# Performance work log

Hardware: AMD Instinct MI355X
Metric: run time of the kernel (lower is better)

Reference implementation:

```python
import jax, jax.numpy as jnp
import numpy as np

B, S, H = 2, 2048, 1024
NH, HD = 16, 64  # num heads, head dim
EPS = 1e-12


def setup_inputs() -> dict:
    key = jax.random.key(0)
    ks = jax.random.split(key, 10)
    sc = 1.0 / np.sqrt(H)
    return {
        "hidden_states": jax.random.normal(ks[0], (B, S, H), jnp.float32),
        "Wq": jax.random.normal(ks[1], (H, H), jnp.float32) * sc,
        "bq": jnp.zeros((H,), jnp.float32),
        "Wk": jax.random.normal(ks[2], (H, H), jnp.float32) * sc,
        "bk": jnp.zeros((H,), jnp.float32),
        "Wv": jax.random.normal(ks[3], (H, H), jnp.float32) * sc,
        "bv": jnp.zeros((H,), jnp.float32),
        "Wo": jax.random.normal(ks[4], (H, H), jnp.float32) * sc,
        "bo": jnp.zeros((H,), jnp.float32),
        "ln_g": jnp.ones((H,), jnp.float32),
        "ln_b": jnp.zeros((H,), jnp.float32),
    }


def reference(hidden_states, Wq, bq, Wk, bk, Wv, bv, Wo, bo, ln_g, ln_b):
    x = hidden_states  # [B,S,H]
    def split_heads(t):
        return t.reshape(B, S, NH, HD).transpose(0, 2, 1, 3)  # [B,NH,S,HD]
    q = split_heads(x @ Wq.T + bq)
    k = split_heads(x @ Wk.T + bk)
    v = split_heads(x @ Wv.T + bv)
    scores = jnp.einsum("bhqd,bhkd->bhqk", q, k) / np.sqrt(HD)
    causal = jnp.tril(jnp.ones((S, S), bool))  # [S,S]
    scores = jnp.where(causal[None, None], scores, -jnp.inf)
    probs = jax.nn.softmax(scores, axis=-1)
    ctx = jnp.einsum("bhqk,bhkd->bhqd", probs, v)
    ctx = ctx.transpose(0, 2, 1, 3).reshape(B, S, H)
    attn_out = ctx @ Wo.T + bo
    y = attn_out + x
    mu = jnp.mean(y, axis=-1, keepdims=True)
    var = jnp.mean((y - mu) ** 2, axis=-1, keepdims=True)
    return (y - mu) / jnp.sqrt(var + EPS) * ln_g + ln_b
```

## Files before the change

### kernel.cpp

```cpp
#include <hip/hip_runtime.h>

#define B_  2
#define S_  2048
#define H_  1024
#define NH_ 16
#define HD_ 64
#define M_  (B_*S_)

typedef __attribute__((ext_vector_type(8))) __bf16 bf16x8;
typedef __attribute__((ext_vector_type(4))) float  f32x4;
typedef __attribute__((ext_vector_type(8))) unsigned short us8;
typedef __attribute__((ext_vector_type(4))) float  fl4;

#define GL16(g, l) __builtin_amdgcn_global_load_lds( \
    (const __attribute__((address_space(1))) unsigned int*)(g), \
    (__attribute__((address_space(3))) unsigned int*)(l), 16, 0, 0)

__device__ __forceinline__ unsigned short f2bf(float f) {
    unsigned int u = __float_as_uint(f);
    u += 0x7fffu + ((u >> 16) & 1u);
    return (unsigned short)(u >> 16);
}

__global__ __launch_bounds__(256) void cast_kernel(
    const float* __restrict__ x,
    const float* __restrict__ wq, const float* __restrict__ wk,
    const float* __restrict__ wv, const float* __restrict__ wo,
    unsigned short* __restrict__ xb, unsigned short* __restrict__ wb) {
    size_t t  = (size_t)blockIdx.x * 256 + threadIdx.x;
    size_t e0 = t * 4;
    const size_t XN = (size_t)M_ * H_;
    const float* src;
    unsigned short* dst;
    if (e0 < XN) { src = x + e0; dst = xb + e0; }
    else {
        size_t j = e0 - XN;
        int w = (int)(j >> 20);
        size_t off = j & ((1u << 20) - 1);
        const float* wp = (w == 0) ? wq : (w == 1) ? wk : (w == 2) ? wv : wo;
        src = wp + off; dst = wb + j;
    }
    fl4 v = *(const fl4*)src;
    ushort4 o;
    o.x = f2bf(v.x); o.y = f2bf(v.y); o.z = f2bf(v.z); o.w = f2bf(v.w);
    *(ushort4*)dst = o;
}

__global__ __launch_bounds__(256) void gemm_qkv(
    const unsigned short* __restrict__ xb, const unsigned short* __restrict__ wb,
    const float* __restrict__ bq, const float* __restrict__ bk,
    const float* __restrict__ bv,
    unsigned short* __restrict__ qb, unsigned short* __restrict__ kbuf,
    unsigned short* __restrict__ vT) {
    __shared__ __align__(16) unsigned short As[128 * 64];
    __shared__ __align__(16) unsigned short Bs[128 * 64];
    const int z = blockIdx.z;
    const unsigned short* W = wb + ((size_t)z << 20);
    const int m0 = blockIdx.x * 128, n0 = blockIdx.y * 128;
    const int t = threadIdx.x, lane = t & 63, w = t >> 6;
    const int wm = w >> 1, wn = w & 1, quad = lane >> 4, l16 = lane & 15;
    const int srow = w * 32 + (lane >> 3);
    const int scol = (lane & 7) * 8;
    const unsigned short* ga = xb + (size_t)(m0 + srow) * H_ + scol;
    const unsigned short* gb = W  + (size_t)(n0 + srow) * H_ + scol;

    f32x4 acc[4][4] = {};
    for (int k0 = 0; k0 < H_; k0 += 64) {
        __syncthreads();
#pragma unroll
        for (int j = 0; j < 4; j++) {
            GL16(ga + (size_t)(j * 8) * H_ + k0, &As[(w * 32 + j * 8) * 64]);
            GL16(gb + (size_t)(j * 8) * H_ + k0, &Bs[(w * 32 + j * 8) * 64]);
        }
        __syncthreads();
#pragma unroll
        for (int kk = 0; kk < 64; kk += 32) {
            bf16x8 af[4], bfr[4];
#pragma unroll
            for (int i = 0; i < 4; i++)
                af[i]  = *(const bf16x8*)&As[(wm * 64 + i * 16 + l16) * 64 + kk + quad * 8];
#pragma unroll
            for (int i = 0; i < 4; i++)
                bfr[i] = *(const bf16x8*)&Bs[(wn * 64 + i * 16 + l16) * 64 + kk + quad * 8];
#pragma unroll
            for (int mi = 0; mi < 4; mi++)
#pragma unroll
                for (int ni = 0; ni < 4; ni++)
                    acc[mi][ni] = __builtin_amdgcn_mfma_f32_16x16x32_bf16(
                        af[mi], bfr[ni], acc[mi][ni], 0, 0, 0);
        }
    }
    const float* bias = (z == 0) ? bq : (z == 1) ? bk : bv;
    if (z == 2) {
#pragma unroll
        for (int mi = 0; mi < 4; mi++) {
#pragma unroll
            for (int ni = 0; ni < 4; ni++) {
                int col  = n0 + wn * 64 + ni * 16 + l16;
                float bval = bias[col];
                int row0 = m0 + wm * 64 + mi * 16 + quad * 4;
                int bb = row0 >> 11, s0 = row0 & 2047;
                ushort4 pk;
                pk.x = f2bf(acc[mi][ni][0] + bval);
                pk.y = f2bf(acc[mi][ni][1] + bval);
                pk.z = f2bf(acc[mi][ni][2] + bval);
                pk.w = f2bf(acc[mi][ni][3] + bval);
                *(ushort4*)&vT[((size_t)bb * NH_ * HD_ + col) * S_ + s0] = pk;
            }
        }
    } else {
        unsigned short* out = (z == 0) ? qb : kbuf;
        const float qs = (z == 0) ? 0.18033688f : 1.0f;
#pragma unroll
        for (int mi = 0; mi < 4; mi++) {
#pragma unroll
            for (int ni = 0; ni < 4; ni++) {
                int col = n0 + wn * 64 + ni * 16 + l16;
                float bval = bias[col];
#pragma unroll
                for (int r = 0; r < 4; r++) {
                    int row = m0 + wm * 64 + mi * 16 + quad * 4 + r;
                    out[(size_t)row * H_ + col] = f2bf((acc[mi][ni][r] + bval) * qs);
                }
            }
        }
    }
}

__global__ __launch_bounds__(256) void gemm_out(
    const unsigned short* __restrict__ ctxb, const unsigned short* __restrict__ wob,
    const float* __restrict__ bo, const float* __restrict__ x,
    float* __restrict__ y) {
    __shared__ __align__(16) unsigned short As[128 * 64];
    __shared__ __align__(16) unsigned short Bs[64 * 64];
    const int m0 = blockIdx.x * 128, n0 = blockIdx.y * 64;
    const int t = threadIdx.x, lane = t & 63, w = t >> 6;
    const int quad = lane >> 4, l16 = lane & 15;
    const int l8r = lane >> 3, l8c = (lane & 7) * 8;
    const unsigned short* ga = ctxb + (size_t)(m0 + w * 32 + l8r) * H_ + l8c;
    const unsigned short* gb = wob  + (size_t)(n0 + w * 16 + l8r) * H_ + l8c;

    f32x4 acc[2][4] = {};
    for (int k0 = 0; k0 < H_; k0 += 64) {
        __syncthreads();
#pragma unroll
        for (int j = 0; j < 4; j++)
            GL16(ga + (size_t)(j * 8) * H_ + k0, &As[(w * 32 + j * 8) * 64]);
#pragma unroll
        for (int j = 0; j < 2; j++)
            GL16(gb + (size_t)(j * 8) * H_ + k0, &Bs[(w * 16 + j * 8) * 64]);
        __syncthreads();
#pragma unroll
        for (int kk = 0; kk < 64; kk += 32) {
            bf16x8 af[2], bfr[4];
#pragma unroll
            for (int i = 0; i < 2; i++)
                af[i]  = *(const bf16x8*)&As[(w * 32 + i * 16 + l16) * 64 + kk + quad * 8];
#pragma unroll
            for (int i = 0; i < 4; i++)
                bfr[i] = *(const bf16x8*)&Bs[(i * 16 + l16) * 64 + kk + quad * 8];
#pragma unroll
            for (int mi = 0; mi < 2; mi++)
#pragma unroll
                for (int ni = 0; ni < 4; ni++)
                    acc[mi][ni] = __builtin_amdgcn_mfma_f32_16x16x32_bf16(
                        af[mi], bfr[ni], acc[mi][ni], 0, 0, 0);
        }
    }
#pragma unroll
    for (int mi = 0; mi < 2; mi++) {
#pragma unroll
        for (int ni = 0; ni < 4; ni++) {
            int col = n0 + ni * 16 + l16;
            float bval = bo[col];
#pragma unroll
            for (int r = 0; r < 4; r++) {
                size_t idx = (size_t)(m0 + w * 32 + mi * 16 + quad * 4 + r) * H_ + col;
                y[idx] = acc[mi][ni][r] + bval + x[idx];
            }
        }
    }
}

__global__ __launch_bounds__(256) void attn_kernel(
    const unsigned short* __restrict__ qb, const unsigned short* __restrict__ kb,
    const unsigned short* __restrict__ vT, unsigned short* __restrict__ ctxb) {
    __shared__ __align__(16) unsigned short Ks[2][64 * 72];
    __shared__ __align__(16) unsigned short Vt[2][64 * 72];
    __shared__ __align__(16) unsigned short Ps[64 * 76];
    const int flat = blockIdx.x + (blockIdx.y << 4) + (blockIdx.z << 8);
    const int xcd = flat & 7, slot = flat >> 3;
    const int bh = xcd * 4 + (slot >> 4);
    const int p  = slot & 15;
    const int b = bh >> 4, h = bh & 15;
    const int t = threadIdx.x, lane = t & 63, wid = t >> 6;
    const int quad = lane >> 4, l16 = lane & 15;
    const int sr = t >> 2, sc = (t & 3) * 16;
    const size_t headoff = (size_t)h * HD_;
    const unsigned short* vtb = vT + ((size_t)(b * NH_ + h) * HD_) * S_;

    for (int half = 0; half < 2; half++) {
        const int qt = half ? (31 - p) : p;
        const int q0 = qt * 64;
        const size_t qrow = (size_t)(b * S_ + q0 + wid * 16 + l16);
        bf16x8 qf0 = *(const bf16x8*)(qb + qrow * H_ + headoff + quad * 8);
        bf16x8 qf1 = *(const bf16x8*)(qb + qrow * H_ + headoff + 32 + quad * 8);

        float m_r = -1e30f, l_r = 0.f;
        f32x4 o_acc[4] = {};

        const unsigned short* kptr = kb  + (size_t)(b * S_ + sr) * H_ + headoff + sc;
        const unsigned short* vptr = vtb + (size_t)sr * S_ + sc;
        us8 nk0 = *(const us8*)(kptr);
        us8 nk1 = *(const us8*)(kptr + 8);
        us8 nv0 = *(const us8*)(vptr);
        us8 nv1 = *(const us8*)(vptr + 8);
        __syncthreads();
        *(us8*)&Ks[0][sr * 72 + sc]     = nk0;  *(us8*)&Ks[0][sr * 72 + sc + 8] = nk1;
        *(us8*)&Vt[0][sr * 72 + sc]     = nv0;  *(us8*)&Vt[0][sr * 72 + sc + 8] = nv1;
        __syncthreads();

        for (int s = 0; s <= qt; s++) {
            const int buf = s & 1;
            const bool pf = (s < qt);
            if (pf) {
                kptr += (size_t)64 * H_;
                vptr += 64;
                nk0 = *(const us8*)(kptr);
                nk1 = *(const us8*)(kptr + 8);
                nv0 = *(const us8*)(vptr);
                nv1 = *(const us8*)(vptr + 8);
            }
            f32x4 sacc[4] = {};
#pragma unroll
            for (int kk = 0; kk < 64; kk += 32) {
                bf16x8 bq_ = (kk == 0) ? qf0 : qf1;
#pragma unroll
                for (int nt = 0; nt < 4; nt++) {
                    bf16x8 ak = *(const bf16x8*)&Ks[buf][(nt * 16 + l16) * 72 + kk + quad * 8];
                    sacc[nt] = __builtin_amdgcn_mfma_f32_16x16x32_bf16(ak, bq_, sacc[nt], 0, 0, 0);
                }
            }
            if (s == qt) {
#pragma unroll
                for (int nt = 0; nt < 4; nt++) {
#pragma unroll
                    for (int r = 0; r < 4; r++) {
                        int key = nt * 16 + quad * 4 + r;
                        if (key > wid * 16 + l16) sacc[nt][r] = -1e30f;
                    }
                }
            }
            float mx = sacc[0][0];
#pragma unroll
            for (int nt = 0; nt < 4; nt++)
#pragma unroll
                for (int r = 0; r < 4; r++) mx = fmaxf(mx, sacc[nt][r]);
            mx = fmaxf(mx, __shfl_xor(mx, 16));
            mx = fmaxf(mx, __shfl_xor(mx, 32));
            float m_new = fmaxf(m_r, mx);
            float alpha = exp2f(m_r - m_new);
            float ss = 0.f;
#pragma unroll
            for (int nt = 0; nt < 4; nt++) {
                ushort4 pk;
                float p0 = exp2f(sacc[nt][0] - m_new);
                float p1 = exp2f(sacc[nt][1] - m_new);
                float p2 = exp2f(sacc[nt][2] - m_new);
                float p3 = exp2f(sacc[nt][3] - m_new);
                ss += (p0 + p1) + (p2 + p3);
                pk.x = (unsigned short)(__float_as_uint(p0) >> 16);
                pk.y = (unsigned short)(__float_as_uint(p1) >> 16);
                pk.z = (unsigned short)(__float_as_uint(p2) >> 16);
                pk.w = (unsigned short)(__float_as_uint(p3) >> 16);
                *(ushort4*)&Ps[(wid * 16 + l16) * 76 + nt * 16 + quad * 4] = pk;
            }
            ss += __shfl_xor(ss, 16);
            ss += __shfl_xor(ss, 32);
            l_r = l_r * alpha + ss;
            m_r = m_new;
#pragma unroll
            for (int dt = 0; dt < 4; dt++)
#pragma unroll
                for (int r = 0; r < 4; r++) o_acc[dt][r] *= alpha;
            __threadfence_block();
#pragma unroll
            for (int kk = 0; kk < 64; kk += 32) {
                bf16x8 pfr = *(const bf16x8*)&Ps[(wid * 16 + l16) * 76 + kk + quad * 8];
#pragma unroll
                for (int dt = 0; dt < 4; dt++) {
                    bf16x8 vf = *(const bf16x8*)&Vt[buf][(dt * 16 + l16) * 72 + kk + quad * 8];
                    o_acc[dt] = __builtin_amdgcn_mfma_f32_16x16x32_bf16(vf, pfr, o_acc[dt], 0, 0, 0);
                }
            }
            if (pf) {
                *(us8*)&Ks[buf ^ 1][sr * 72 + sc]     = nk0;
                *(us8*)&Ks[buf ^ 1][sr * 72 + sc + 8] = nk1;
                *(us8*)&Vt[buf ^ 1][sr * 72 + sc]     = nv0;
                *(us8*)&Vt[buf ^ 1][sr * 72 + sc + 8] = nv1;
                __syncthreads();
            }
        }
        {
            float inv = 1.0f / l_r;
            size_t row = (size_t)(b * S_ + q0 + wid * 16 + l16);
#pragma unroll
            for (int dt = 0; dt < 4; dt++) {
                ushort4 pk;
                pk.x = f2bf(o_acc[dt][0] * inv);
                pk.y = f2bf(o_acc[dt][1] * inv);
                pk.z = f2bf(o_acc[dt][2] * inv);
                pk.w = f2bf(o_acc[dt][3] * inv);
                *(ushort4*)&ctxb[row * H_ + headoff + dt * 16 + quad * 4] = pk;
            }
        }
    }
}

__global__ __launch_bounds__(256) void ln_kernel(
    const float* __restrict__ y, const float* __restrict__ g,
    const float* __restrict__ bta, float* __restrict__ out) {
    __shared__ float red[8];
    const int row = blockIdx.x, t = threadIdx.x;
    fl4 v = *(const fl4*)(y + (size_t)row * H_ + t * 4);
    float s  = v.x + v.y + v.z + v.w;
    float sq = v.x * v.x + v.y * v.y + v.z * v.z + v.w * v.w;
    for (int m = 1; m < 64; m <<= 1) { s += __shfl_xor(s, m); sq += __shfl_xor(sq, m); }
    const int wid = t >> 6, lane = t & 63;
    if (lane == 0) { red[wid * 2] = s; red[wid * 2 + 1] = sq; }
    __syncthreads();
    s  = red[0] + red[2] + red[4] + red[6];
    sq = red[1] + red[3] + red[5] + red[7];
    float mu   = s * (1.0f / H_);
    float var  = sq * (1.0f / H_) - mu * mu;
    float rstd = rsqrtf(fmaxf(var, 0.f) + 1e-12f);
    fl4 gg = *(const fl4*)(g + t * 4);
    fl4 bb = *(const fl4*)(bta + t * 4);
    fl4 o;
    o.x = (v.x - mu) * rstd * gg.x + bb.x;
    o.y = (v.y - mu) * rstd * gg.y + bb.y;
    o.z = (v.z - mu) * rstd * gg.z + bb.z;
    o.w = (v.w - mu) * rstd * gg.w + bb.w;
    *(fl4*)(out + (size_t)row * H_ + t * 4) = o;
}

extern "C" void kernel_launch(void* const* d_in, const int* in_sizes, int n_in,
                              void* d_out, int out_size, void* d_ws, size_t ws_size,
                              hipStream_t stream) {
    const float* x  = (const float*)d_in[0];
    const float* Wq = (const float*)d_in[1];
    const float* bq = (const float*)d_in[2];
    const float* Wk = (const float*)d_in[3];
    const float* bk = (const float*)d_in[4];
    const float* Wv = (const float*)d_in[5];
    const float* bv = (const float*)d_in[6];
    const float* Wo = (const float*)d_in[7];
    const float* bo = (const float*)d_in[8];
    const float* lg = (const float*)d_in[9];
    const float* lb = (const float*)d_in[10];
    float* out = (float*)d_out;

    const size_t MEG = 1024u * 1024u;
    unsigned short* ws16 = (unsigned short*)d_ws;
    unsigned short* xb   = ws16;
    unsigned short* wb   = ws16 + 4 * MEG;
    unsigned short* qb   = ws16 + 8 * MEG;
    unsigned short* kb   = ws16 + 12 * MEG;
    unsigned short* vT   = ws16 + 16 * MEG;
    unsigned short* ctxb = ws16 + 20 * MEG;
    float* y = (float*)(ws16 + 24 * MEG);

    cast_kernel<<<8192, 256, 0, stream>>>(x, Wq, Wk, Wv, Wo, xb, wb);
    gemm_qkv<<<dim3(32, 8, 3), 256, 0, stream>>>(xb, wb, bq, bk, bv, qb, kb, vT);
    attn_kernel<<<dim3(16, 16, 2), 256, 0, stream>>>(qb, kb, vT, ctxb);
    gemm_out<<<dim3(32, 16), 256, 0, stream>>>(ctxb, wb + 3 * MEG, bo, x, y);
    ln_kernel<<<4096, 256, 0, stream>>>(y, lg, lb, out);
}
```

Baseline: 216.5 us.

## Share each K/V tile stream across four query tiles in larger attention blocks

The attention kernel now runs 512-thread blocks. Each block handles four causal query tiles: two warp groups, each owning a front tile and its mirrored back tile. All 32 K/V tiles are streamed once per block and reused by every query tile that still needs them, where before each 64-row query tile re-read K/V on its own. The aim is to cut global K/V traffic and per-tile barrier overhead. The cost is that each warp now holds two sets of accumulators, which raises register pressure, and the grid shrinks to 256 blocks, lowering scheduling flexibility.

```diff
diff --git a/kernel.cpp b/kernel.cpp
--- a/kernel.cpp
+++ b/kernel.cpp
@@ -182,63 +182,69 @@
     }
 }
 
-__global__ __launch_bounds__(256) void attn_kernel(
+__global__ __launch_bounds__(512, 4) void attn_kernel(
     const unsigned short* __restrict__ qb, const unsigned short* __restrict__ kb,
     const unsigned short* __restrict__ vT, unsigned short* __restrict__ ctxb) {
     __shared__ __align__(16) unsigned short Ks[2][64 * 72];
     __shared__ __align__(16) unsigned short Vt[2][64 * 72];
-    __shared__ __align__(16) unsigned short Ps[64 * 76];
-    const int flat = blockIdx.x + (blockIdx.y << 4) + (blockIdx.z << 8);
+    __shared__ __align__(16) unsigned short Ps[128 * 76];
+    const int flat = blockIdx.x;
     const int xcd = flat & 7, slot = flat >> 3;
-    const int bh = xcd * 4 + (slot >> 4);
-    const int p  = slot & 15;
+    const int bh  = xcd * 4 + (slot >> 3);
+    const int j   = slot & 7;
     const int b = bh >> 4, h = bh & 15;
     const int t = threadIdx.x, lane = t & 63, wid = t >> 6;
+    const int grp = wid >> 2, wid4 = wid & 3;
     const int quad = lane >> 4, l16 = lane & 15;
-    const int sr = t >> 2, sc = (t & 3) * 16;
+    const int sr8 = t >> 3, sc8 = (t & 7) * 8;
     const size_t headoff = (size_t)h * HD_;
     const unsigned short* vtb = vT + ((size_t)(b * NH_ + h) * HD_) * S_;
 
-    for (int half = 0; half < 2; half++) {
-        const int qt = half ? (31 - p) : p;
-        const int q0 = qt * 64;
-        const size_t qrow = (size_t)(b * S_ + q0 + wid * 16 + l16);
-        bf16x8 qf0 = *(const bf16x8*)(qb + qrow * H_ + headoff + quad * 8);
-        bf16x8 qf1 = *(const bf16x8*)(qb + qrow * H_ + headoff + 32 + quad * 8);
-
-        float m_r = -1e30f, l_r = 0.f;
-        f32x4 o_acc[4] = {};
-
-        const unsigned short* kptr = kb  + (size_t)(b * S_ + sr) * H_ + headoff + sc;
-        const unsigned short* vptr = vtb + (size_t)sr * S_ + sc;
-        us8 nk0 = *(const us8*)(kptr);
-        us8 nk1 = *(const us8*)(kptr + 8);
-        us8 nv0 = *(const us8*)(vptr);
-        us8 nv1 = *(const us8*)(vptr + 8);
-        __syncthreads();
-        *(us8*)&Ks[0][sr * 72 + sc]     = nk0;  *(us8*)&Ks[0][sr * 72 + sc + 8] = nk1;
-        *(us8*)&Vt[0][sr * 72 + sc]     = nv0;  *(us8*)&Vt[0][sr * 72 + sc + 8] = nv1;
-        __syncthreads();
-
-        for (int s = 0; s <= qt; s++) {
-            const int buf = s & 1;
-            const bool pf = (s < qt);
-            if (pf) {
-                kptr += (size_t)64 * H_;
-                vptr += 64;
-                nk0 = *(const us8*)(kptr);
-                nk1 = *(const us8*)(kptr + 8);
-                nv0 = *(const us8*)(vptr);
-                nv1 = *(const us8*)(vptr + 8);
-            }
+    const int p   = j * 2 + grp;
+    const int qt1 = p, qt2 = 31 - p;
+    const int q01 = qt1 * 64, q02 = qt2 * 64;
+
+    const size_t qr1 = (size_t)(b * S_ + q01 + wid4 * 16 + l16);
+    const size_t qr2 = (size_t)(b * S_ + q02 + wid4 * 16 + l16);
+    bf16x8 q1a = *(const bf16x8*)(qb + qr1 * H_ + headoff + quad * 8);
+    bf16x8 q1b = *(const bf16x8*)(qb + qr1 * H_ + headoff + 32 + quad * 8);
+    bf16x8 q2a = *(const bf16x8*)(qb + qr2 * H_ + headoff + quad * 8);
+    bf16x8 q2b = *(const bf16x8*)(qb + qr2 * H_ + headoff + 32 + quad * 8);
+
+    float m1 = -1e30f, l1 = 0.f, m2 = -1e30f, l2 = 0.f;
+    f32x4 o1[4] = {}, o2[4] = {};
+
+    const unsigned short* kptr = kb  + (size_t)(b * S_ + sr8) * H_ + headoff + sc8;
+    const unsigned short* vptr = vtb + (size_t)sr8 * S_ + sc8;
+    us8 nk = *(const us8*)kptr;
+    us8 nv = *(const us8*)vptr;
+    *(us8*)&Ks[0][sr8 * 72 + sc8] = nk;
+    *(us8*)&Vt[0][sr8 * 72 + sc8] = nv;
+    __syncthreads();
+
+    for (int s = 0; s < 32; s++) {
+        const int buf = s & 1;
+        const bool pf = (s < 31);
+        if (pf) {
+            kptr += (size_t)64 * H_;
+            vptr += 64;
+            nk = *(const us8*)kptr;
+            nv = *(const us8*)vptr;
+        }
+#pragma unroll
+        for (int tile = 0; tile < 2; tile++) {
+            const int  qt  = tile ? qt2 : qt1;
+            if (s > qt) continue;
+            const bf16x8 qa = tile ? q2a : q1a;
+            const bf16x8 qb_ = tile ? q2b : q1b;
             f32x4 sacc[4] = {};
 #pragma unroll
             for (int kk = 0; kk < 64; kk += 32) {
-                bf16x8 bq_ = (kk == 0) ? qf0 : qf1;
+                bf16x8 bqf = (kk == 0) ? qa : qb_;
 #pragma unroll
                 for (int nt = 0; nt < 4; nt++) {
                     bf16x8 ak = *(const bf16x8*)&Ks[buf][(nt * 16 + l16) * 72 + kk + quad * 8];
-                    sacc[nt] = __builtin_amdgcn_mfma_f32_16x16x32_bf16(ak, bq_, sacc[nt], 0, 0, 0);
+                    sacc[nt] = __builtin_amdgcn_mfma_f32_16x16x32_bf16(ak, bqf, sacc[nt], 0, 0, 0);
                 }
             }
             if (s == qt) {
@@ -247,7 +253,7 @@
 #pragma unroll
                     for (int r = 0; r < 4; r++) {
                         int key = nt * 16 + quad * 4 + r;
-                        if (key > wid * 16 + l16) sacc[nt][r] = -1e30f;
+                        if (key > wid4 * 16 + l16) sacc[nt][r] = -1e30f;
                     }
                 }
             }
@@ -258,8 +264,9 @@
                 for (int r = 0; r < 4; r++) mx = fmaxf(mx, sacc[nt][r]);
             mx = fmaxf(mx, __shfl_xor(mx, 16));
             mx = fmaxf(mx, __shfl_xor(mx, 32));
-            float m_new = fmaxf(m_r, mx);
-            float alpha = exp2f(m_r - m_new);
+            float m_old = tile ? m2 : m1;
+            float m_new = fmaxf(m_old, mx);
+            float alpha = exp2f(m_old - m_new);
             float ss = 0.f;
 #pragma unroll
             for (int nt = 0; nt < 4; nt++) {
@@ -277,12 +284,13 @@
             }
             ss += __shfl_xor(ss, 16);
             ss += __shfl_xor(ss, 32);
-            l_r = l_r * alpha + ss;
-            m_r = m_new;
+            if (tile) { l2 = l2 * alpha + ss; m2 = m_new; }
+            else      { l1 = l1 * alpha + ss; m1 = m_new; }
+            f32x4* oo = tile ? o2 : o1;
 #pragma unroll
             for (int dt = 0; dt < 4; dt++)
 #pragma unroll
-                for (int r = 0; r < 4; r++) o_acc[dt][r] *= alpha;
+                for (int r = 0; r < 4; r++) oo[dt][r] *= alpha;
             __threadfence_block();
 #pragma unroll
             for (int kk = 0; kk < 64; kk += 32) {
@@ -290,29 +298,30 @@
 #pragma unroll
                 for (int dt = 0; dt < 4; dt++) {
                     bf16x8 vf = *(const bf16x8*)&Vt[buf][(dt * 16 + l16) * 72 + kk + quad * 8];
-                    o_acc[dt] = __builtin_amdgcn_mfma_f32_16x16x32_bf16(vf, pfr, o_acc[dt], 0, 0, 0);
+                    oo[dt] = __builtin_amdgcn_mfma_f32_16x16x32_bf16(vf, pfr, oo[dt], 0, 0, 0);
                 }
             }
-            if (pf) {
-                *(us8*)&Ks[buf ^ 1][sr * 72 + sc]     = nk0;
-                *(us8*)&Ks[buf ^ 1][sr * 72 + sc + 8] = nk1;
-                *(us8*)&Vt[buf ^ 1][sr * 72 + sc]     = nv0;
-                *(us8*)&Vt[buf ^ 1][sr * 72 + sc + 8] = nv1;
-                __syncthreads();
-            }
-        }
-        {
-            float inv = 1.0f / l_r;
-            size_t row = (size_t)(b * S_ + q0 + wid * 16 + l16);
-#pragma unroll
-            for (int dt = 0; dt < 4; dt++) {
-                ushort4 pk;
-                pk.x = f2bf(o_acc[dt][0] * inv);
-                pk.y = f2bf(o_acc[dt][1] * inv);
-                pk.z = f2bf(o_acc[dt][2] * inv);
-                pk.w = f2bf(o_acc[dt][3] * inv);
-                *(ushort4*)&ctxb[row * H_ + headoff + dt * 16 + quad * 4] = pk;
-            }
+        }
+        if (pf) {
+            *(us8*)&Ks[buf ^ 1][sr8 * 72 + sc8] = nk;
+            *(us8*)&Vt[buf ^ 1][sr8 * 72 + sc8] = nv;
+            __syncthreads();
+        }
+    }
+#pragma unroll
+    for (int tile = 0; tile < 2; tile++) {
+        const int q0 = tile ? q02 : q01;
+        const float inv = 1.0f / (tile ? l2 : l1);
+        const f32x4* oo = tile ? o2 : o1;
+        size_t row = (size_t)(b * S_ + q0 + wid4 * 16 + l16);
+#pragma unroll
+        for (int dt = 0; dt < 4; dt++) {
+            ushort4 pk;
+            pk.x = f2bf(oo[dt][0] * inv);
+            pk.y = f2bf(oo[dt][1] * inv);
+            pk.z = f2bf(oo[dt][2] * inv);
+            pk.w = f2bf(oo[dt][3] * inv);
+            *(ushort4*)&ctxb[row * H_ + headoff + dt * 16 + quad * 4] = pk;
         }
     }
 }
@@ -372,7 +381,7 @@
 
     cast_kernel<<<8192, 256, 0, stream>>>(x, Wq, Wk, Wv, Wo, xb, wb);
     gemm_qkv<<<dim3(32, 8, 3), 256, 0, stream>>>(xb, wb, bq, bk, bv, qb, kb, vT);
-    attn_kernel<<<dim3(16, 16, 2), 256, 0, stream>>>(qb, kb, vT, ctxb);
+    attn_kernel<<<dim3(256), 512, 0, stream>>>(qb, kb, vT, ctxb);
     gemm_out<<<dim3(32, 16), 256, 0, stream>>>(ctxb, wb + 3 * MEG, bo, x, y);
     ln_kernel<<<4096, 256, 0, stream>>>(y, lg, lb, out);
 }
```

Result: no change. 217.1 us (+0.3%).
